# Kernel optimization log

Measured on AMD Instinct MI355X. Metric: run time of the kernel, lower is better.

The kernel has to match this reference:

```python
import jax, jax.numpy as jnp
import numpy as np

DIM = 1024
FFN = 4096
E = 10      # num_domains
N = 8192    # tokens
STEPS = 1   # GatedMLP steps (depth=1 layer)


def gated_mlp(x, W1, b1, W2, b2, Wg, bg):
    # depth=1, steps=STEPS; dropout=0 (eval). Residual MLP block with sigmoid gate.
    h = x
    for _ in range(STEPS):
        h = jax.nn.gelu(h @ W1 + b1, approximate=False) @ W2 + b2 + h
    g = jax.nn.sigmoid(x @ Wg + bg)
    return g * h + (1.0 - g) * x


def setup_inputs() -> dict:
    key = jax.random.key(0)
    ks = jax.random.split(key, 16)
    s1 = 1.0 / np.sqrt(DIM)
    s2 = 1.0 / np.sqrt(FFN)
    inp = {
        "x": jax.random.normal(ks[0], (N, DIM), dtype=jnp.float32),
        "domain_ids": jax.random.randint(ks[1], (N,), 0, E, dtype=jnp.int32),
        # shared expert
        "sW1": jax.random.normal(ks[2], (DIM, FFN), dtype=jnp.float32) * s1,
        "sb1": jnp.zeros((FFN,), dtype=jnp.float32),
        "sW2": jax.random.normal(ks[3], (FFN, DIM), dtype=jnp.float32) * s2,
        "sb2": jnp.zeros((DIM,), dtype=jnp.float32),
        "sWg": jax.random.normal(ks[4], (DIM, DIM), dtype=jnp.float32) * (0.01 * s1),
        "sbg": jnp.full((DIM,), -4.0, dtype=jnp.float32),
        # domain experts, stacked over E
        "dW1": jax.random.normal(ks[5], (E, DIM, FFN), dtype=jnp.float32) * s1,
        "db1": jnp.zeros((E, FFN), dtype=jnp.float32),
        "dW2": jax.random.normal(ks[6], (E, FFN, DIM), dtype=jnp.float32) * s2,
        "db2": jnp.zeros((E, DIM), dtype=jnp.float32),
        "dWg": jax.random.normal(ks[7], (E, DIM, DIM), dtype=jnp.float32) * (0.01 * s1),
        "dbg": jnp.full((E, DIM), -4.0, dtype=jnp.float32),
    }
    return inp


def reference(x, domain_ids, sW1, sb1, sW2, sb2, sWg, sbg,
              dW1, db1, dW2, db2, dWg, dbg):
    out = gated_mlp(x, sW1, sb1, sW2, sb2, sWg, sbg)
    # each token belongs to exactly one domain expert; dense dispatch via mask
    for e in range(E):
        mask = (domain_ids == e).astype(x.dtype)[:, None]  # [N,1]
        expert_out = gated_mlp(x, dW1[e], db1[e], dW2[e], db2[e], dWg[e], dbg[e])
        out = out + mask * expert_out
    return out
```

## Files before the change

kernel.cpp:

```cpp
#include <hip/hip_runtime.h>
#include <hip/hip_bf16.h>
#include <math.h>

#define NTOK 8192
#define DIM  1024
#define FFN  4096
#define NEXP 10

#define NT_SH (NTOK / 128)
#define NT_RT (NTOK / 128 + NEXP - 1)
#define NY01  ((FFN + DIM) / 128)
#define NY2   (DIM / 128)

typedef __attribute__((ext_vector_type(8))) short bf16x8;
typedef __attribute__((ext_vector_type(4))) float f32x4;

static __device__ __forceinline__ unsigned short f2bf(float f) {
  __hip_bfloat16 h = __float2bfloat16(f);
  return *reinterpret_cast<unsigned short*>(&h);
}

static __device__ __forceinline__ void gld_lds16(const unsigned short* g, unsigned short* l) {
  __builtin_amdgcn_global_load_lds((const __attribute__((address_space(1))) unsigned int*)g,
                                   (__attribute__((address_space(3))) unsigned int*)l,
                                   16, 0, 0);
}

template <int NX, int NY, int G>
static __device__ __forceinline__ void map_block(int orig, int& bx, int& by) {
  const int n = NX * NY;
  int xcd = orig & 7, o = orig >> 3;
  const int q = n >> 3, r = n & 7;
  int id = (xcd < r ? xcd * (q + 1) : r * (q + 1) + (xcd - r) * q) + o;
  const int gsz = NX * G;
  int grp = id / gsz;
  int rem = id - grp * gsz;
  bx = rem / G;
  by = grp * G + (rem - bx * G);
}

__global__ void k_zero(int* cnt) { if (threadIdx.x < NEXP) cnt[threadIdx.x] = 0; }

__global__ void k_count(const int* __restrict__ dom, int* __restrict__ cnt, int* __restrict__ pos) {
  int t = blockIdx.x * 256 + threadIdx.x;
  if (t < NTOK) pos[t] = atomicAdd(&cnt[dom[t]], 1);
}

__global__ void k_offsets(const int* __restrict__ cnt, int* __restrict__ segoff,
                          int* __restrict__ tilemap, int* __restrict__ ntiles) {
  if (threadIdx.x == 0) {
    int s = 0, k = 0;
    for (int e = 0; e < NEXP; e++) {
      segoff[e] = s;
      int c = cnt[e];
      int nt = (c + 127) >> 7;
      for (int t = 0; t < nt; t++) tilemap[k++] = (e << 16) | t;
      s += c;
    }
    segoff[NEXP] = s;
    *ntiles = k;
  }
}

__global__ void k_scatter(const int* __restrict__ dom, const int* __restrict__ pos,
                          const int* __restrict__ segoff, int* __restrict__ perm) {
  int t = blockIdx.x * 256 + threadIdx.x;
  if (t < NTOK) perm[segoff[dom[t]] + pos[t]] = t;
}

__global__ void k_convert(const float* __restrict__ src, unsigned short* __restrict__ dst, int n8) {
  int i = blockIdx.x * 256 + threadIdx.x;
  if (i >= n8) return;
  const float4* s = (const float4*)(src + (size_t)i * 8);
  float4 a = s[0], b = s[1];
  union { unsigned short h[8]; uint4 v; } u;
  u.h[0] = f2bf(a.x); u.h[1] = f2bf(a.y); u.h[2] = f2bf(a.z); u.h[3] = f2bf(a.w);
  u.h[4] = f2bf(b.x); u.h[5] = f2bf(b.y); u.h[6] = f2bf(b.z); u.h[7] = f2bf(b.w);
  *(uint4*)(dst + (size_t)i * 8) = u.v;
}

__global__ void k_gather(const unsigned short* __restrict__ xb, const int* __restrict__ perm,
                         unsigned short* __restrict__ xs) {
  int i = blockIdx.x * 256 + threadIdx.x;
  int row = i >> 7;
  int c = (i & 127) * 8;
  int src = perm[row];
  *(uint4*)(xs + (size_t)row * DIM + c) = *(const uint4*)(xb + (size_t)src * DIM + c);
}

__global__ void k_transpose(const float* __restrict__ src, unsigned short* __restrict__ dst,
                            int K, int N) {
  size_t moff = (size_t)blockIdx.z * K * N;
  src += moff; dst += moff;
  __shared__ float tile[64][65];
  int n0 = blockIdx.x * 64, k0 = blockIdx.y * 64;
  int t = threadIdx.x;
  int tx = t & 15, ty = t >> 4;
#pragma unroll
  for (int i = 0; i < 4; i++) {
    int kk = ty + i * 16;
    float4 v = *(const float4*)(src + (size_t)(k0 + kk) * N + n0 + tx * 4);
    tile[kk][tx * 4 + 0] = v.x; tile[kk][tx * 4 + 1] = v.y;
    tile[kk][tx * 4 + 2] = v.z; tile[kk][tx * 4 + 3] = v.w;
  }
  __syncthreads();
#pragma unroll
  for (int i = 0; i < 2; i++) {
    int chunk = t + i * 256;
    int nl = chunk >> 3;
    int k8 = (chunk & 7) * 8;
    union { unsigned short h[8]; uint4 v; } u;
#pragma unroll
    for (int j = 0; j < 8; j++) u.h[j] = f2bf(tile[k8 + j][nl]);
    *(uint4*)(dst + (size_t)(n0 + nl) * K + k0 + k8) = u.v;
  }
}

static __device__ __forceinline__ void mfma_tile(
    const unsigned short* gA0, const unsigned short* gA1,
    const unsigned short* gB0, const unsigned short* gB1,
    unsigned short (*As)[32], unsigned short (*Bs)[32],
    int w, int lane, int K, f32x4 acc[4][4])
{
  unsigned short* lA0 = &As[0][0] + w * 1024;
  unsigned short* lA1 = lA0 + 512;
  unsigned short* lB0 = &Bs[0][0] + w * 1024;
  unsigned short* lB1 = lB0 + 512;
  int m16 = lane & 15, kh = (lane >> 4) * 8;
  int wr = (w >> 1) * 64, wc = (w & 1) * 64;
  for (int kt = 0; kt < K; kt += 32) {
    gld_lds16(gA0, lA0); gld_lds16(gA1, lA1);
    gld_lds16(gB0, lB0); gld_lds16(gB1, lB1);
    gA0 += 32; gA1 += 32; gB0 += 32; gB1 += 32;
    __syncthreads();
    bf16x8 af[4], bfr[4];
#pragma unroll
    for (int i = 0; i < 4; i++) af[i] = *(const bf16x8*)&As[wr + i * 16 + m16][kh];
#pragma unroll
    for (int j = 0; j < 4; j++) bfr[j] = *(const bf16x8*)&Bs[wc + j * 16 + m16][kh];
#pragma unroll
    for (int i = 0; i < 4; i++)
#pragma unroll
      for (int j = 0; j < 4; j++)
        acc[i][j] = __builtin_amdgcn_mfma_f32_16x16x32_bf16(af[i], bfr[j], acc[i][j], 0, 0, 0);
    __syncthreads();
  }
}

template <bool ROUTED>
__global__ __launch_bounds__(256)
void k_gemm01(const unsigned short* __restrict__ A,
              const unsigned short* __restrict__ W1t,
              const float* __restrict__ b1,
              const unsigned short* __restrict__ Wgt,
              const float* __restrict__ bg,
              unsigned short* __restrict__ h1,
              float* __restrict__ g,
              const int* __restrict__ segoff,
              const int* __restrict__ tilemap,
              const int* __restrict__ ntilesp) {
  constexpr int NX = ROUTED ? NT_RT : NT_SH;
  int bx, by;
  map_block<NX, NY01, 8>((int)blockIdx.x, bx, by);

  int e = 0, seg0 = 0, cnt = NTOK, m0;
  if (ROUTED) {
    if (bx >= *ntilesp) return;
    int tm = tilemap[bx];
    e = tm >> 16;
    seg0 = segoff[e];
    cnt = segoff[e + 1] - seg0;
    m0 = (tm & 0xffff) << 7;
  } else {
    m0 = bx << 7;
  }

  const bool isW1 = by < (FFN / 128);
  const int n0 = (isW1 ? by : by - FFN / 128) << 7;
  const unsigned short* Bte = isW1 ? W1t + (size_t)e * FFN * DIM + (size_t)n0 * DIM
                                   : Wgt + (size_t)e * DIM * DIM + (size_t)n0 * DIM;
  const float* be = (isW1 ? b1 + (size_t)e * FFN : bg + (size_t)e * DIM) + n0;

  __shared__ unsigned short As[128][32];
  __shared__ unsigned short Bs[128][32];

  int tid = threadIdx.x, w = tid >> 6, lane = tid & 63;
  int p0 = w * 128 + lane;
  int r0 = p0 >> 2, r1 = r0 + 16;
  int kc = (p0 & 3) * 8;

  auto arow = [&](int rl) -> size_t {
    int l = m0 + rl;
    if (ROUTED && l > cnt - 1) l = cnt - 1;
    return (size_t)(seg0 + l);
  };
  const unsigned short* gA0 = A + arow(r0) * DIM + kc;
  const unsigned short* gA1 = A + arow(r1) * DIM + kc;
  const unsigned short* gB0 = Bte + (size_t)r0 * DIM + kc;
  const unsigned short* gB1 = Bte + (size_t)r1 * DIM + kc;

  f32x4 acc[4][4];
#pragma unroll
  for (int i = 0; i < 4; i++)
#pragma unroll
    for (int j = 0; j < 4; j++) acc[i][j] = (f32x4){0.f, 0.f, 0.f, 0.f};

  mfma_tile(gA0, gA1, gB0, gB1, As, Bs, w, lane, DIM, acc);

  int m16 = lane & 15, quad = lane >> 4;
  int wr = (w >> 1) * 64, wc = (w & 1) * 64;
#pragma unroll
  for (int i = 0; i < 4; i++) {
#pragma unroll
    for (int j = 0; j < 4; j++) {
      int cn = wc + j * 16 + m16;
      int col = n0 + cn;
#pragma unroll
      for (int r = 0; r < 4; r++) {
        int rl = wr + i * 16 + quad * 4 + r;
        int l = m0 + rl;
        if (ROUTED && l >= cnt) continue;
        float z = acc[i][j][r] + be[cn];
        size_t row = (size_t)(seg0 + l);
        if (isW1) {
          z = 0.5f * z * (1.0f + erff(z * 0.70710678118654752f));
          h1[row * FFN + col] = f2bf(z);
        } else {
          z = 1.0f / (1.0f + expf(-z));
          g[row * DIM + col] = z;
        }
      }
    }
  }
}

template <bool ROUTED>
__global__ __launch_bounds__(256)
void k_gemm2(const unsigned short* __restrict__ A,
             const unsigned short* __restrict__ W2t,
             const float* __restrict__ b2,
             const float* __restrict__ g,
             const float* __restrict__ xres,
             float* __restrict__ out,
             const int* __restrict__ perm,
             const int* __restrict__ segoff,
             const int* __restrict__ tilemap,
             const int* __restrict__ ntilesp) {
  constexpr int NX = ROUTED ? NT_RT : NT_SH;
  int bx, by;
  map_block<NX, NY2, 2>((int)blockIdx.x, bx, by);

  int e = 0, seg0 = 0, cnt = NTOK, m0;
  if (ROUTED) {
    if (bx >= *ntilesp) return;
    int tm = tilemap[bx];
    e = tm >> 16;
    seg0 = segoff[e];
    cnt = segoff[e + 1] - seg0;
    m0 = (tm & 0xffff) << 7;
  } else {
    m0 = bx << 7;
  }
  const int n0 = by << 7;
  const unsigned short* Bte = W2t + (size_t)e * DIM * FFN + (size_t)n0 * FFN;
  const float* be = b2 + (size_t)e * DIM + n0;

  __shared__ unsigned short As[128][32];
  __shared__ unsigned short Bs[128][32];

  int tid = threadIdx.x, w = tid >> 6, lane = tid & 63;
  int p0 = w * 128 + lane;
  int r0 = p0 >> 2, r1 = r0 + 16;
  int kc = (p0 & 3) * 8;

  auto arow = [&](int rl) -> size_t {
    int l = m0 + rl;
    if (ROUTED && l > cnt - 1) l = cnt - 1;
    return (size_t)(seg0 + l);
  };
  const unsigned short* gA0 = A + arow(r0) * FFN + kc;
  const unsigned short* gA1 = A + arow(r1) * FFN + kc;
  const unsigned short* gB0 = Bte + (size_t)r0 * FFN + kc;
  const unsigned short* gB1 = Bte + (size_t)r1 * FFN + kc;

  f32x4 acc[4][4];
#pragma unroll
  for (int i = 0; i < 4; i++)
#pragma unroll
    for (int j = 0; j < 4; j++) acc[i][j] = (f32x4){0.f, 0.f, 0.f, 0.f};

  mfma_tile(gA0, gA1, gB0, gB1, As, Bs, w, lane, FFN, acc);

  int m16 = lane & 15, quad = lane >> 4;
  int wr = (w >> 1) * 64, wc = (w & 1) * 64;
#pragma unroll
  for (int i = 0; i < 4; i++) {
#pragma unroll
    for (int j = 0; j < 4; j++) {
      int cn = wc + j * 16 + m16;
      int col = n0 + cn;
#pragma unroll
      for (int r = 0; r < 4; r++) {
        int rl = wr + i * 16 + quad * 4 + r;
        int l = m0 + rl;
        if (ROUTED && l >= cnt) continue;
        int lidx = seg0 + l;
        int grow = ROUTED ? perm[lidx] : l;
        float xv = xres[(size_t)grow * DIM + col];
        float gv = g[(size_t)lidx * DIM + col];
        float h = acc[i][j][r] + be[cn] + xv;
        float o = gv * h + (1.0f - gv) * xv;
        float* po = &out[(size_t)grow * DIM + col];
        if (ROUTED) *po += o;
        else        *po = o;
      }
    }
  }
}

extern "C" void kernel_launch(void* const* d_in, const int* in_sizes, int n_in,
                              void* d_out, int out_size, void* d_ws, size_t ws_size,
                              hipStream_t stream) {
  (void)in_sizes; (void)n_in; (void)out_size; (void)ws_size;
  const float* x   = (const float*)d_in[0];
  const int*   dom = (const int*)d_in[1];
  const float* sW1 = (const float*)d_in[2];
  const float* sb1 = (const float*)d_in[3];
  const float* sW2 = (const float*)d_in[4];
  const float* sb2 = (const float*)d_in[5];
  const float* sWg = (const float*)d_in[6];
  const float* sbg = (const float*)d_in[7];
  const float* dW1 = (const float*)d_in[8];
  const float* db1 = (const float*)d_in[9];
  const float* dW2 = (const float*)d_in[10];
  const float* db2 = (const float*)d_in[11];
  const float* dWg = (const float*)d_in[12];
  const float* dbg = (const float*)d_in[13];
  float* out = (float*)d_out;

  char* p = (char*)d_ws;
  auto take = [&](size_t b) { char* r = p; p += (b + 255) & ~(size_t)255; return r; };
  int* cnt     = (int*)take(NEXP * 4);
  int* segoff  = (int*)take((NEXP + 1) * 4);
  int* tilemap = (int*)take(128 * 4);
  int* ntiles  = (int*)take(4);
  int* pos     = (int*)take((size_t)NTOK * 4);
  int* perm    = (int*)take((size_t)NTOK * 4);
  unsigned short* xb   = (unsigned short*)take((size_t)NTOK * DIM * 2);
  unsigned short* xs   = (unsigned short*)take((size_t)NTOK * DIM * 2);
  unsigned short* h1   = (unsigned short*)take((size_t)NTOK * FFN * 2);
  float*          g    = (float*)take((size_t)NTOK * DIM * 4);
  unsigned short* sW1t = (unsigned short*)take((size_t)DIM * FFN * 2);
  unsigned short* sW2t = (unsigned short*)take((size_t)FFN * DIM * 2);
  unsigned short* sWgt = (unsigned short*)take((size_t)DIM * DIM * 2);
  unsigned short* dW1t = (unsigned short*)take((size_t)NEXP * DIM * FFN * 2);
  unsigned short* dW2t = (unsigned short*)take((size_t)NEXP * FFN * DIM * 2);
  unsigned short* dWgt = (unsigned short*)take((size_t)NEXP * DIM * DIM * 2);

  k_zero<<<1, 64, 0, stream>>>(cnt);
  k_count<<<NTOK / 256, 256, 0, stream>>>(dom, cnt, pos);
  k_offsets<<<1, 1, 0, stream>>>(cnt, segoff, tilemap, ntiles);
  k_scatter<<<NTOK / 256, 256, 0, stream>>>(dom, pos, segoff, perm);

  k_convert<<<(NTOK * DIM / 8) / 256, 256, 0, stream>>>(x, xb, NTOK * DIM / 8);
  k_gather<<<(NTOK * DIM / 8) / 256, 256, 0, stream>>>(xb, perm, xs);
  k_transpose<<<dim3(FFN / 64, DIM / 64, 1),    256, 0, stream>>>(sW1, sW1t, DIM, FFN);
  k_transpose<<<dim3(DIM / 64, FFN / 64, 1),    256, 0, stream>>>(sW2, sW2t, FFN, DIM);
  k_transpose<<<dim3(DIM / 64, DIM / 64, 1),    256, 0, stream>>>(sWg, sWgt, DIM, DIM);
  k_transpose<<<dim3(FFN / 64, DIM / 64, NEXP), 256, 0, stream>>>(dW1, dW1t, DIM, FFN);
  k_transpose<<<dim3(DIM / 64, FFN / 64, NEXP), 256, 0, stream>>>(dW2, dW2t, FFN, DIM);
  k_transpose<<<dim3(DIM / 64, DIM / 64, NEXP), 256, 0, stream>>>(dWg, dWgt, DIM, DIM);

  k_gemm01<false><<<NT_SH * NY01, 256, 0, stream>>>(
      xb, sW1t, sb1, sWgt, sbg, h1, g, nullptr, nullptr, nullptr);
  k_gemm2<false><<<NT_SH * NY2, 256, 0, stream>>>(
      h1, sW2t, sb2, g, x, out, nullptr, nullptr, nullptr, nullptr);

  k_gemm01<true><<<NT_RT * NY01, 256, 0, stream>>>(
      xs, dW1t, db1, dWgt, dbg, h1, g, segoff, tilemap, ntiles);
  k_gemm2<true><<<NT_RT * NY2, 256, 0, stream>>>(
      h1, dW2t, db2, g, x, out, perm, segoff, tilemap, ntiles);
}
```

Before: 1.143 ms.

## Double-buffer LDS tiles with XOR swizzle, fuse convert/gather, use tanh GELU

The GEMM main loop now double-buffers its LDS tiles so the next K-slice loads while MFMAs run on the current one. An XOR swizzle on the k-chunk cuts LDS bank conflicts, and the loop uses one barrier per step instead of two. The x conversion and routed gather are fused into one kernel that writes both the natural and the permuted bf16 copies, and per-column bias loads are hoisted. GELU switches from exact erf to a tanh approximation with fast exp, which changes numerics slightly relative to the exact reference.

```diff
diff --git a/kernel.cpp b/kernel.cpp
--- a/kernel.cpp
+++ b/kernel.cpp
@@ -24,6 +24,11 @@
   __builtin_amdgcn_global_load_lds((const __attribute__((address_space(1))) unsigned int*)g,
                                    (__attribute__((address_space(3))) unsigned int*)l,
                                    16, 0, 0);
+}
+
+template <int N>
+static __device__ __forceinline__ void waitv() {
+  asm volatile("s_waitcnt vmcnt(%0)" :: "i"(N) : "memory");
 }
 
 template <int NX, int NY, int G>
@@ -53,8 +58,7 @@
     for (int e = 0; e < NEXP; e++) {
       segoff[e] = s;
       int c = cnt[e];
-      int nt = (c + 127) >> 7;
-      for (int t = 0; t < nt; t++) tilemap[k++] = (e << 16) | t;
+      for (int t = 0; t < ((c + 127) >> 7); t++) tilemap[k++] = (e << 16) | t;
       s += c;
     }
     segoff[NEXP] = s;
@@ -68,24 +72,20 @@
   if (t < NTOK) perm[segoff[dom[t]] + pos[t]] = t;
 }
 
-__global__ void k_convert(const float* __restrict__ src, unsigned short* __restrict__ dst, int n8) {
+__global__ void k_convert_g(const float* __restrict__ src, const int* __restrict__ dom,
+                            const int* __restrict__ pos, const int* __restrict__ segoff,
+                            unsigned short* __restrict__ xb, unsigned short* __restrict__ xs) {
   int i = blockIdx.x * 256 + threadIdx.x;
-  if (i >= n8) return;
-  const float4* s = (const float4*)(src + (size_t)i * 8);
+  int row = i >> 7;
+  int c = (i & 127) * 8;
+  const float4* s = (const float4*)(src + (size_t)row * DIM + c);
   float4 a = s[0], b = s[1];
   union { unsigned short h[8]; uint4 v; } u;
   u.h[0] = f2bf(a.x); u.h[1] = f2bf(a.y); u.h[2] = f2bf(a.z); u.h[3] = f2bf(a.w);
   u.h[4] = f2bf(b.x); u.h[5] = f2bf(b.y); u.h[6] = f2bf(b.z); u.h[7] = f2bf(b.w);
-  *(uint4*)(dst + (size_t)i * 8) = u.v;
-}
-
-__global__ void k_gather(const unsigned short* __restrict__ xb, const int* __restrict__ perm,
-                         unsigned short* __restrict__ xs) {
-  int i = blockIdx.x * 256 + threadIdx.x;
-  int row = i >> 7;
-  int c = (i & 127) * 8;
-  int src = perm[row];
-  *(uint4*)(xs + (size_t)row * DIM + c) = *(const uint4*)(xb + (size_t)src * DIM + c);
+  *(uint4*)(xb + (size_t)row * DIM + c) = u.v;
+  int srow = segoff[dom[row]] + pos[row];
+  *(uint4*)(xs + (size_t)srow * DIM + c) = u.v;
 }
 
 __global__ void k_transpose(const float* __restrict__ src, unsigned short* __restrict__ dst,
@@ -119,31 +119,43 @@
 static __device__ __forceinline__ void mfma_tile(
     const unsigned short* gA0, const unsigned short* gA1,
     const unsigned short* gB0, const unsigned short* gB1,
-    unsigned short (*As)[32], unsigned short (*Bs)[32],
-    int w, int lane, int K, f32x4 acc[4][4])
+    unsigned short (*As)[128][32], unsigned short (*Bs)[128][32],
+    int tid, int K, f32x4 acc[4][4])
 {
-  unsigned short* lA0 = &As[0][0] + w * 1024;
-  unsigned short* lA1 = lA0 + 512;
-  unsigned short* lB0 = &Bs[0][0] + w * 1024;
-  unsigned short* lB1 = lB0 + 512;
-  int m16 = lane & 15, kh = (lane >> 4) * 8;
+  int w = tid >> 6, lane = tid & 63;
+  int p0 = w * 128 + lane;
+  int m16 = lane & 15;
+  int kslot = (lane >> 4) ^ ((m16 >> 1) & 3);
   int wr = (w >> 1) * 64, wc = (w & 1) * 64;
-  for (int kt = 0; kt < K; kt += 32) {
-    gld_lds16(gA0, lA0); gld_lds16(gA1, lA1);
-    gld_lds16(gB0, lB0); gld_lds16(gB1, lB1);
+
+  auto stage = [&](int b) {
+    unsigned short* la = &As[b][0][0] + p0 * 8;
+    unsigned short* lb = &Bs[b][0][0] + p0 * 8;
+    gld_lds16(gA0, la); gld_lds16(gA1, la + 512);
+    gld_lds16(gB0, lb); gld_lds16(gB1, lb + 512);
     gA0 += 32; gA1 += 32; gB0 += 32; gB1 += 32;
-    __syncthreads();
+  };
+
+  stage(0);
+  waitv<0>();
+  __builtin_amdgcn_s_barrier();
+
+  int nsteps = K >> 5;
+  for (int s = 0; s < nsteps; ++s) {
+    int cur = s & 1;
+    if (s + 1 < nsteps) stage(cur ^ 1);
     bf16x8 af[4], bfr[4];
 #pragma unroll
-    for (int i = 0; i < 4; i++) af[i] = *(const bf16x8*)&As[wr + i * 16 + m16][kh];
-#pragma unroll
-    for (int j = 0; j < 4; j++) bfr[j] = *(const bf16x8*)&Bs[wc + j * 16 + m16][kh];
+    for (int i = 0; i < 4; i++) af[i] = *(const bf16x8*)&As[cur][wr + i * 16 + m16][kslot * 8];
+#pragma unroll
+    for (int j = 0; j < 4; j++) bfr[j] = *(const bf16x8*)&Bs[cur][wc + j * 16 + m16][kslot * 8];
 #pragma unroll
     for (int i = 0; i < 4; i++)
 #pragma unroll
       for (int j = 0; j < 4; j++)
         acc[i][j] = __builtin_amdgcn_mfma_f32_16x16x32_bf16(af[i], bfr[j], acc[i][j], 0, 0, 0);
-    __syncthreads();
+    waitv<0>();
+    __builtin_amdgcn_s_barrier();
   }
 }
 
@@ -181,23 +193,23 @@
                                    : Wgt + (size_t)e * DIM * DIM + (size_t)n0 * DIM;
   const float* be = (isW1 ? b1 + (size_t)e * FFN : bg + (size_t)e * DIM) + n0;
 
-  __shared__ unsigned short As[128][32];
-  __shared__ unsigned short Bs[128][32];
+  __shared__ unsigned short As[2][128][32];
+  __shared__ unsigned short Bs[2][128][32];
 
   int tid = threadIdx.x, w = tid >> 6, lane = tid & 63;
   int p0 = w * 128 + lane;
   int r0 = p0 >> 2, r1 = r0 + 16;
-  int kc = (p0 & 3) * 8;
+  int kgx = ((p0 & 3) ^ ((p0 >> 3) & 3)) * 8;
 
   auto arow = [&](int rl) -> size_t {
     int l = m0 + rl;
     if (ROUTED && l > cnt - 1) l = cnt - 1;
     return (size_t)(seg0 + l);
   };
-  const unsigned short* gA0 = A + arow(r0) * DIM + kc;
-  const unsigned short* gA1 = A + arow(r1) * DIM + kc;
-  const unsigned short* gB0 = Bte + (size_t)r0 * DIM + kc;
-  const unsigned short* gB1 = Bte + (size_t)r1 * DIM + kc;
+  const unsigned short* gA0 = A + arow(r0) * DIM + kgx;
+  const unsigned short* gA1 = A + arow(r1) * DIM + kgx;
+  const unsigned short* gB0 = Bte + (size_t)r0 * DIM + kgx;
+  const unsigned short* gB1 = Bte + (size_t)r1 * DIM + kgx;
 
   f32x4 acc[4][4];
 #pragma unroll
@@ -205,7 +217,7 @@
 #pragma unroll
     for (int j = 0; j < 4; j++) acc[i][j] = (f32x4){0.f, 0.f, 0.f, 0.f};
 
-  mfma_tile(gA0, gA1, gB0, gB1, As, Bs, w, lane, DIM, acc);
+  mfma_tile(gA0, gA1, gB0, gB1, As, Bs, tid, DIM, acc);
 
   int m16 = lane & 15, quad = lane >> 4;
   int wr = (w >> 1) * 64, wc = (w & 1) * 64;
@@ -215,19 +227,20 @@
     for (int j = 0; j < 4; j++) {
       int cn = wc + j * 16 + m16;
       int col = n0 + cn;
+      float bb = be[cn];
 #pragma unroll
       for (int r = 0; r < 4; r++) {
         int rl = wr + i * 16 + quad * 4 + r;
         int l = m0 + rl;
         if (ROUTED && l >= cnt) continue;
-        float z = acc[i][j][r] + be[cn];
+        float z = acc[i][j][r] + bb;
         size_t row = (size_t)(seg0 + l);
         if (isW1) {
-          z = 0.5f * z * (1.0f + erff(z * 0.70710678118654752f));
-          h1[row * FFN + col] = f2bf(z);
+          float u = 0.79788456f * z * (1.0f + 0.044715f * z * z);
+          float o = z / (1.0f + __expf(-2.0f * u));
+          h1[row * (size_t)FFN + col] = f2bf(o);
         } else {
-          z = 1.0f / (1.0f + expf(-z));
-          g[row * DIM + col] = z;
+          g[row * (size_t)DIM + col] = 1.0f / (1.0f + __expf(-z));
         }
       }
     }
@@ -265,23 +278,23 @@
   const unsigned short* Bte = W2t + (size_t)e * DIM * FFN + (size_t)n0 * FFN;
   const float* be = b2 + (size_t)e * DIM + n0;
 
-  __shared__ unsigned short As[128][32];
-  __shared__ unsigned short Bs[128][32];
+  __shared__ unsigned short As[2][128][32];
+  __shared__ unsigned short Bs[2][128][32];
 
   int tid = threadIdx.x, w = tid >> 6, lane = tid & 63;
   int p0 = w * 128 + lane;
   int r0 = p0 >> 2, r1 = r0 + 16;
-  int kc = (p0 & 3) * 8;
+  int kgx = ((p0 & 3) ^ ((p0 >> 3) & 3)) * 8;
 
   auto arow = [&](int rl) -> size_t {
     int l = m0 + rl;
     if (ROUTED && l > cnt - 1) l = cnt - 1;
     return (size_t)(seg0 + l);
   };
-  const unsigned short* gA0 = A + arow(r0) * FFN + kc;
-  const unsigned short* gA1 = A + arow(r1) * FFN + kc;
-  const unsigned short* gB0 = Bte + (size_t)r0 * FFN + kc;
-  const unsigned short* gB1 = Bte + (size_t)r1 * FFN + kc;
+  const unsigned short* gA0 = A + arow(r0) * FFN + kgx;
+  const unsigned short* gA1 = A + arow(r1) * FFN + kgx;
+  const unsigned short* gB0 = Bte + (size_t)r0 * FFN + kgx;
+  const unsigned short* gB1 = Bte + (size_t)r1 * FFN + kgx;
 
   f32x4 acc[4][4];
 #pragma unroll
@@ -289,7 +302,7 @@
 #pragma unroll
     for (int j = 0; j < 4; j++) acc[i][j] = (f32x4){0.f, 0.f, 0.f, 0.f};
 
-  mfma_tile(gA0, gA1, gB0, gB1, As, Bs, w, lane, FFN, acc);
+  mfma_tile(gA0, gA1, gB0, gB1, As, Bs, tid, FFN, acc);
 
   int m16 = lane & 15, quad = lane >> 4;
   int wr = (w >> 1) * 64, wc = (w & 1) * 64;
@@ -299,6 +312,7 @@
     for (int j = 0; j < 4; j++) {
       int cn = wc + j * 16 + m16;
       int col = n0 + cn;
+      float bb = be[cn];
 #pragma unroll
       for (int r = 0; r < 4; r++) {
         int rl = wr + i * 16 + quad * 4 + r;
@@ -308,7 +322,7 @@
         int grow = ROUTED ? perm[lidx] : l;
         float xv = xres[(size_t)grow * DIM + col];
         float gv = g[(size_t)lidx * DIM + col];
-        float h = acc[i][j][r] + be[cn] + xv;
+        float h = acc[i][j][r] + bb + xv;
         float o = gv * h + (1.0f - gv) * xv;
         float* po = &out[(size_t)grow * DIM + col];
         if (ROUTED) *po += o;
@@ -362,8 +376,7 @@
   k_offsets<<<1, 1, 0, stream>>>(cnt, segoff, tilemap, ntiles);
   k_scatter<<<NTOK / 256, 256, 0, stream>>>(dom, pos, segoff, perm);
 
-  k_convert<<<(NTOK * DIM / 8) / 256, 256, 0, stream>>>(x, xb, NTOK * DIM / 8);
-  k_gather<<<(NTOK * DIM / 8) / 256, 256, 0, stream>>>(xb, perm, xs);
+  k_convert_g<<<(NTOK * DIM / 8) / 256, 256, 0, stream>>>(x, dom, pos, segoff, xb, xs);
   k_transpose<<<dim3(FFN / 64, DIM / 64, 1),    256, 0, stream>>>(sW1, sW1t, DIM, FFN);
   k_transpose<<<dim3(DIM / 64, FFN / 64, 1),    256, 0, stream>>>(sW2, sW2t, FFN, DIM);
   k_transpose<<<dim3(DIM / 64, DIM / 64, 1),    256, 0, stream>>>(sWg, sWgt, DIM, DIM);
```

After: 1.184 ms. 1.04x slower.
